# Performance work log

Hardware: AMD Instinct MI355X
Metric: run time of the kernel (lower is better)

Reference implementation:

```python
import jax, jax.numpy as jnp
import numpy as np

OUT_FEATURES = 4096
IN_FEATURES = 4096
GROUP_SIZE = 128
NUM_GROUPS = IN_FEATURES // GROUP_SIZE  # 32
PACKED_SIZE = OUT_FEATURES * IN_FEATURES // 8  # 2097152


def setup_inputs() -> dict:
    key = jax.random.key(0)
    k1, k2, k3, k4 = jax.random.split(key, 4)
    x = jax.random.normal(k1, (2, 512, IN_FEATURES), dtype=jnp.float32)
    # random packed 4-bit weights (8 nibbles per int32)
    w_packed = jax.random.randint(k2, (PACKED_SIZE,), jnp.iinfo(jnp.int32).min,
                                  jnp.iinfo(jnp.int32).max, dtype=jnp.int32)
    w_scale = jax.random.uniform(k3, (OUT_FEATURES, NUM_GROUPS), dtype=jnp.float32) * 0.05
    w_zero = jax.random.randint(k4, (OUT_FEATURES, NUM_GROUPS), 0, 8, dtype=jnp.int32)
    return {"x": x, "w_packed": w_packed, "w_scale": w_scale, "w_zero": w_zero}


def _unpack_dequant(w_packed, w_scale, w_zero):
    # Extract 8 nibbles per int32: (v >> (i*4)) & 0xF, i = 0..7
    shifts = jnp.arange(8, dtype=jnp.int32) * 4
    nibbles = (w_packed[:, None] >> shifts[None, :]) & 15  # [packed, 8]
    w4 = nibbles.reshape(-1)  # [out*in], values 0..15
    w4 = jnp.where(w4 >= 8, w4 - 16, w4)  # signed 4-bit -> [-8, 7]
    w_int = w4.reshape(OUT_FEATURES, NUM_GROUPS, GROUP_SIZE).astype(jnp.float32)
    # per-(row, group) dequant: (q - zero) * scale
    w = (w_int - w_zero[:, :, None].astype(jnp.float32)) * w_scale[:, :, None]
    return w.reshape(OUT_FEATURES, IN_FEATURES)


def reference(x, w_packed, w_scale, w_zero):
    weight = _unpack_dequant(w_packed, w_scale, w_zero).astype(x.dtype)
    # F.linear: y = x @ W^T
    return jnp.einsum('bsi,oi->bso', x, weight)
```

## Files before the change

### kernel.cpp

```cpp
#include <hip/hip_runtime.h>
#include <stdint.h>

#define IN_F 4096
#define OUT_F 4096
#define NG 32
#define NSTEP 32

typedef __attribute__((ext_vector_type(8))) _Float16 half8;
typedef __attribute__((ext_vector_type(2))) _Float16 half2t;
typedef __attribute__((ext_vector_type(4))) float floatx4;

__device__ __forceinline__ unsigned pkh(float a, float b) {
  return __builtin_bit_cast(unsigned, __builtin_amdgcn_cvt_pkrtz(a, b));
}

__global__ __launch_bounds__(256) void prep_kernel(
    const float* __restrict__ x, _Float16* __restrict__ Xh,
    const float* __restrict__ wscale, const int* __restrict__ wzero,
    uint2* __restrict__ SZ, int nxb) {
  int b = blockIdx.x;
  if (b < nxb) {
    int i = b * 256 + threadIdx.x;
    const float4* x4 = (const float4*)x;
    float4 a = x4[2 * i];
    float4 c = x4[2 * i + 1];
    uint4 o;
    o.x = pkh(a.x, c.x);
    o.y = pkh(a.y, c.y);
    o.z = pkh(a.z, c.z);
    o.w = pkh(a.w, c.w);
    ((uint4*)Xh)[i] = o;
  } else {
    int i = (b - nxb) * 256 + threadIdx.x;
    float s = wscale[i];
    int zp = wzero[i];
    _Float16 sh = (_Float16)s;
    _Float16 ch = (_Float16)(float)(1032 + zp);
    unsigned s2 = (unsigned)__builtin_bit_cast(unsigned short, sh) * 0x10001u;
    unsigned c2 = (unsigned)__builtin_bit_cast(unsigned short, ch) * 0x10001u;
    SZ[i] = make_uint2(s2, c2);
  }
}

__device__ __forceinline__ uint4 dequant8(unsigned v, uint2 szv) {
  unsigned tx = v ^ 0x88888888u;
  half2t s2 = __builtin_bit_cast(half2t, szv.x);
  half2t c2 = __builtin_bit_cast(half2t, szv.y);
  unsigned p0 = (tx & 0x000F000Fu) | 0x64006400u;
  unsigned p1 = ((tx >> 4) & 0x000F000Fu) | 0x64006400u;
  unsigned p2 = ((tx >> 8) & 0x000F000Fu) | 0x64006400u;
  unsigned p3 = ((tx >> 12) & 0x000F000Fu) | 0x64006400u;
  half2t w0 = (__builtin_bit_cast(half2t, p0) - c2) * s2;
  half2t w1 = (__builtin_bit_cast(half2t, p1) - c2) * s2;
  half2t w2 = (__builtin_bit_cast(half2t, p2) - c2) * s2;
  half2t w3 = (__builtin_bit_cast(half2t, p3) - c2) * s2;
  uint4 o;
  o.x = __builtin_bit_cast(unsigned, w0);
  o.y = __builtin_bit_cast(unsigned, w1);
  o.z = __builtin_bit_cast(unsigned, w2);
  o.w = __builtin_bit_cast(unsigned, w3);
  return o;
}

__global__ __launch_bounds__(512, 2) void gemm_fused(
    const _Float16* __restrict__ A, const int* __restrict__ wp,
    const uint2* __restrict__ SZ, float* __restrict__ out,
    int M, int N, int K) {
  __shared__ __align__(16) _Float16 Alds[6 * 8192];
  __shared__ __align__(16) _Float16 Blds[4 * 8192];

  const int t = threadIdx.x;
  const int wave = t >> 6, lane = t & 63;
  const int h = wave >> 2, w2 = wave & 3;
  const int wm = (w2 >> 1) * 64, wn = (w2 & 1) * 64;
  const int r = lane & 15, quad = lane >> 4, rb = r & 7;
  const int bm = blockIdx.y * 128, bn = blockIdx.x * 128;

  floatx4 acc[4][4] = {};

  const int kc = t & 7, row0 = t >> 3, row1 = row0 + 64;
  const int gkc = kc ^ (row0 & 7);
  const _Float16* Ag = A + (size_t)bm * K;
  const _Float16* gA[4];
  gA[0] = Ag + (size_t)row0 * K + gkc * 8;
  gA[1] = Ag + (size_t)row1 * K + gkc * 8;
  gA[2] = gA[0] + 2048;
  gA[3] = gA[1] + 2048;

#define STAGE_A(i, st)                                                        \
  {                                                                           \
    _Pragma("unroll") for (int j = 0; j < 4; ++j) {                           \
      const _Float16* src = gA[j] + (i) * 64;                                 \
      int dst = ((st) * 2 + (j >> 1)) * 8192 + (t + 512 * (j & 1)) * 8;       \
      __builtin_amdgcn_global_load_lds(                                       \
          (const __attribute__((address_space(1))) void*)src,                 \
          (__attribute__((address_space(3))) void*)(&Alds[dst]), 16, 0, 0);   \
    }                                                                         \
  }

  const int brow0 = t >> 3, kc8 = t & 7;
  const int* gB0 = wp + (size_t)(bn + brow0) * (IN_F / 8) + kc8;
  const int* gB1 = wp + (size_t)(bn + brow0 + 64) * (IN_F / 8) + kc8;
  const uint2* gS0 = SZ + (size_t)(bn + brow0) * NG;
  const uint2* gS1 = SZ + (size_t)(bn + brow0 + 64) * NG;
  const int bslot0 = brow0 * 64 + ((kc8 ^ (brow0 & 7)) << 3);
  const int bslot1 = (brow0 + 64) * 64 + ((kc8 ^ (brow0 & 7)) << 3);

#define LOADV_B(i, v)                                                         \
  {                                                                           \
    v[0] = (unsigned)gB0[(i) * 8];                                            \
    v[1] = (unsigned)gB1[(i) * 8];                                            \
    v[2] = (unsigned)gB0[(i) * 8 + 256];                                      \
    v[3] = (unsigned)gB1[(i) * 8 + 256];                                      \
  }

#define LOADV_S(g)                                                            \
  {                                                                           \
    sCur[0] = gS0[(g)];                                                       \
    sCur[1] = gS1[(g)];                                                       \
    sCur[2] = gS0[(g) + 16];                                                  \
    sCur[3] = gS1[(g) + 16];                                                  \
  }

#define WRITE_B(v, dstbuf)                                                    \
  {                                                                           \
    _Pragma("unroll") for (int j = 0; j < 4; ++j) {                           \
      int ofs = ((dstbuf) * 2 + (j >> 1)) * 8192 + ((j & 1) ? bslot1 : bslot0); \
      *(uint4*)&Blds[ofs] = dequant8(v[j], sCur[j]);                          \
    }                                                                         \
  }

  unsigned vA[4], vB[4];
  uint2 sCur[4];
  int ra = 0, rw = 2;

  LOADV_B(0, vB);
  LOADV_S(0);
  WRITE_B(vB, 0);
  LOADV_B(1, vA);
  asm volatile("" ::: "memory");
  STAGE_A(0, 0);
  STAGE_A(1, 1);
  asm volatile("s_waitcnt vmcnt(4) lgkmcnt(0)" ::: "memory");
  __builtin_amdgcn_s_barrier();
  __builtin_amdgcn_sched_barrier(0);

#define STEP(i, p, vC, vL, DOSZ, CNTS)                                        \
  {                                                                           \
    if ((i) + 1 < NSTEP) WRITE_B(vC, (p) ^ 1);                                \
    if ((i) + 2 < NSTEP) {                                                    \
      LOADV_B((i) + 2, vL);                                                   \
      if (DOSZ) LOADV_S(((i) + 3) >> 1);                                      \
    }                                                                         \
    asm volatile("" ::: "memory");      \
    if ((i) + 2 < NSTEP) STAGE_A((i) + 2, rw);                                \
    const _Float16* Ab = &Alds[(ra * 2 + h) * 8192];                          \
    const _Float16* Bb = &Blds[((p) * 2 + h) * 8192];                         \
    _Pragma("unroll") for (int ks = 0; ks < 2; ++ks) {                        \
      half8 af[4], bf[4];                                                     \
      _Pragma("unroll") for (int mi = 0; mi < 4; ++mi) {                      \
        int R = wm + mi * 16 + r;                                             \
        af[mi] = *(const half8*)&Ab[R * 64 + (((ks * 4 + quad) ^ rb) << 3)];  \
      }                                                                       \
      _Pragma("unroll") for (int ni = 0; ni < 4; ++ni) {                      \
        int R = wn + ni * 16 + r;                                             \
        bf[ni] = *(const half8*)&Bb[R * 64 + (((ks * 4 + quad) ^ rb) << 3)];  \
      }                                                                       \
      _Pragma("unroll") for (int mi = 0; mi < 4; ++mi)                        \
        _Pragma("unroll") for (int ni = 0; ni < 4; ++ni)                      \
          acc[mi][ni] = __builtin_amdgcn_mfma_f32_16x16x32_f16(               \
              af[mi], bf[ni], acc[mi][ni], 0, 0, 0);                          \
    }                                                                         \
    if ((i) + 2 < NSTEP)                                                      \
      asm volatile("s_waitcnt vmcnt(" CNTS ") lgkmcnt(0)" ::: "memory");      \
    else                                                                      \
      asm volatile("s_waitcnt vmcnt(0) lgkmcnt(0)" ::: "memory");             \
    __builtin_amdgcn_s_barrier();                                             \
    __builtin_amdgcn_sched_barrier(0);                                        \
    ra = (ra + 1 == 3) ? 0 : ra + 1;                                          \
    rw = (rw + 1 == 3) ? 0 : rw + 1;                                          \
  }

  for (int i = 0; i < NSTEP; i += 2) {
    STEP(i, 0, vA, vB, 1, "12");
    STEP(i + 1, 1, vB, vA, 0, "8");
  }

  floatx4* red = (floatx4*)Alds;
  if (h == 1) {
#pragma unroll
    for (int mi = 0; mi < 4; ++mi)
#pragma unroll
      for (int ni = 0; ni < 4; ++ni)
        red[(mi * 4 + ni) * 256 + w2 * 64 + lane] = acc[mi][ni];
  }
  __syncthreads();
  if (h == 0) {
#pragma unroll
    for (int mi = 0; mi < 4; ++mi) {
#pragma unroll
      for (int ni = 0; ni < 4; ++ni) {
        acc[mi][ni] += red[(mi * 4 + ni) * 256 + w2 * 64 + lane];
#pragma unroll
        for (int i = 0; i < 4; ++i) {
          int grow = bm + wm + mi * 16 + quad * 4 + i;
          int gcol = bn + wn + ni * 16 + r;
          out[(size_t)grow * N + gcol] = acc[mi][ni][i];
        }
      }
    }
  }
}

extern "C" void kernel_launch(void* const* d_in, const int* in_sizes, int n_in,
                              void* d_out, int out_size, void* d_ws, size_t ws_size,
                              hipStream_t stream) {
  const float* x = (const float*)d_in[0];
  const int* wp = (const int*)d_in[1];
  const float* wscale = (const float*)d_in[2];
  const int* wzero = (const int*)d_in[3];
  float* out = (float*)d_out;

  int M = in_sizes[0] / IN_F;

  _Float16* Xh = (_Float16*)d_ws;
  uint2* SZ = (uint2*)((char*)d_ws + (size_t)M * IN_F * 2);

  int nxb = (M * IN_F / 8) / 256;
  int nzb = (OUT_F * NG) / 256;
  prep_kernel<<<nxb + nzb, 256, 0, stream>>>(x, Xh, wscale, wzero, SZ, nxb);

  dim3 grid(OUT_F / 128, M / 128);
  gemm_fused<<<grid, 512, 0, stream>>>(Xh, wp, SZ, out, M, OUT_F, IN_F);
}
```

Baseline: 125.8 us.

## Split each K-step into two half-phases with interleaved loads and prioritized MFMA

Each main-loop step is split into two halves. Each half does part of the B dequant write, its LDS fragment loads, part of the global B and A staging, and then 16 MFMAs bracketed by extra barriers and s_setprio(1). This is a ping-pong style schedule meant to overlap memory issue with matrix-core work across waves and raise MFMA priority. It adds two more barriers per step and retunes the vmcnt counts, which risks extra synchronization stalls or subtle ordering errors.

```diff
diff --git a/kernel.cpp b/kernel.cpp
--- a/kernel.cpp
+++ b/kernel.cpp
@@ -87,9 +87,9 @@
   gA[2] = gA[0] + 2048;
   gA[3] = gA[1] + 2048;
 
-#define STAGE_A(i, st)                                                        \
-  {                                                                           \
-    _Pragma("unroll") for (int j = 0; j < 4; ++j) {                           \
+#define STAGE_A_HALF(i, st, hh)                                               \
+  {                                                                           \
+    _Pragma("unroll") for (int j = (hh) * 2; j < (hh) * 2 + 2; ++j) {         \
       const _Float16* src = gA[j] + (i) * 64;                                 \
       int dst = ((st) * 2 + (j >> 1)) * 8192 + (t + 512 * (j & 1)) * 8;       \
       __builtin_amdgcn_global_load_lds(                                       \
@@ -106,14 +106,6 @@
   const int bslot0 = brow0 * 64 + ((kc8 ^ (brow0 & 7)) << 3);
   const int bslot1 = (brow0 + 64) * 64 + ((kc8 ^ (brow0 & 7)) << 3);
 
-#define LOADV_B(i, v)                                                         \
-  {                                                                           \
-    v[0] = (unsigned)gB0[(i) * 8];                                            \
-    v[1] = (unsigned)gB1[(i) * 8];                                            \
-    v[2] = (unsigned)gB0[(i) * 8 + 256];                                      \
-    v[3] = (unsigned)gB1[(i) * 8 + 256];                                      \
-  }
-
 #define LOADV_S(g)                                                            \
   {                                                                           \
     sCur[0] = gS0[(g)];                                                       \
@@ -122,9 +114,9 @@
     sCur[3] = gS1[(g) + 16];                                                  \
   }
 
-#define WRITE_B(v, dstbuf)                                                    \
-  {                                                                           \
-    _Pragma("unroll") for (int j = 0; j < 4; ++j) {                           \
+#define WRITE_B_HALF(v, dstbuf, hh)                                           \
+  {                                                                           \
+    _Pragma("unroll") for (int j = (hh) * 2; j < (hh) * 2 + 2; ++j) {         \
       int ofs = ((dstbuf) * 2 + (j >> 1)) * 8192 + ((j & 1) ? bslot1 : bslot0); \
       *(uint4*)&Blds[ofs] = dequant8(v[j], sCur[j]);                          \
     }                                                                         \
@@ -134,55 +126,97 @@
   uint2 sCur[4];
   int ra = 0, rw = 2;
 
-  LOADV_B(0, vB);
-  LOADV_S(0);
-  WRITE_B(vB, 0);
-  LOADV_B(1, vA);
-  asm volatile("" ::: "memory");
-  STAGE_A(0, 0);
-  STAGE_A(1, 1);
-  asm volatile("s_waitcnt vmcnt(4) lgkmcnt(0)" ::: "memory");
-  __builtin_amdgcn_s_barrier();
-  __builtin_amdgcn_sched_barrier(0);
+  {
+    vB[0] = (unsigned)gB0[0];
+    vB[1] = (unsigned)gB1[0];
+    vB[2] = (unsigned)gB0[256];
+    vB[3] = (unsigned)gB1[256];
+    LOADV_S(0);
+    WRITE_B_HALF(vB, 0, 0);
+    WRITE_B_HALF(vB, 0, 1);
+    vA[0] = (unsigned)gB0[8];
+    vA[1] = (unsigned)gB1[8];
+    vA[2] = (unsigned)gB0[8 + 256];
+    vA[3] = (unsigned)gB1[8 + 256];
+    asm volatile("" ::: "memory");
+    STAGE_A_HALF(0, 0, 0);
+    STAGE_A_HALF(0, 0, 1);
+    STAGE_A_HALF(1, 1, 0);
+    STAGE_A_HALF(1, 1, 1);
+    asm volatile("s_waitcnt vmcnt(4) lgkmcnt(0)" ::: "memory");
+    __builtin_amdgcn_s_barrier();
+    __builtin_amdgcn_sched_barrier(0);
+  }
+
+#define MFMA16(af, bf)                                                        \
+  _Pragma("unroll") for (int mi = 0; mi < 4; ++mi)                            \
+    _Pragma("unroll") for (int ni = 0; ni < 4; ++ni)                          \
+      acc[mi][ni] = __builtin_amdgcn_mfma_f32_16x16x32_f16(                   \
+          af[mi], bf[ni], acc[mi][ni], 0, 0, 0);
 
 #define STEP(i, p, vC, vL, DOSZ, CNTS)                                        \
   {                                                                           \
-    if ((i) + 1 < NSTEP) WRITE_B(vC, (p) ^ 1);                                \
-    if ((i) + 2 < NSTEP) {                                                    \
-      LOADV_B((i) + 2, vL);                                                   \
-      if (DOSZ) LOADV_S(((i) + 3) >> 1);                                      \
-    }                                                                         \
-    asm volatile("" ::: "memory");      \
-    if ((i) + 2 < NSTEP) STAGE_A((i) + 2, rw);                                \
     const _Float16* Ab = &Alds[(ra * 2 + h) * 8192];                          \
     const _Float16* Bb = &Blds[((p) * 2 + h) * 8192];                         \
-    _Pragma("unroll") for (int ks = 0; ks < 2; ++ks) {                        \
-      half8 af[4], bf[4];                                                     \
-      _Pragma("unroll") for (int mi = 0; mi < 4; ++mi) {                      \
-        int R = wm + mi * 16 + r;                                             \
-        af[mi] = *(const half8*)&Ab[R * 64 + (((ks * 4 + quad) ^ rb) << 3)];  \
-      }                                                                       \
-      _Pragma("unroll") for (int ni = 0; ni < 4; ++ni) {                      \
-        int R = wn + ni * 16 + r;                                             \
-        bf[ni] = *(const half8*)&Bb[R * 64 + (((ks * 4 + quad) ^ rb) << 3)];  \
-      }                                                                       \
-      _Pragma("unroll") for (int mi = 0; mi < 4; ++mi)                        \
-        _Pragma("unroll") for (int ni = 0; ni < 4; ++ni)                      \
-          acc[mi][ni] = __builtin_amdgcn_mfma_f32_16x16x32_f16(               \
-              af[mi], bf[ni], acc[mi][ni], 0, 0, 0);                          \
-    }                                                                         \
+                      \
+    if ((i) + 1 < NSTEP) WRITE_B_HALF(vC, (p) ^ 1, 0);                        \
+    half8 af0[4], bf0[4];                                                     \
+    _Pragma("unroll") for (int mi = 0; mi < 4; ++mi) {                        \
+      int R = wm + mi * 16 + r;                                               \
+      af0[mi] = *(const half8*)&Ab[R * 64 + ((quad ^ rb) << 3)];              \
+    }                                                                         \
+    _Pragma("unroll") for (int ni = 0; ni < 4; ++ni) {                        \
+      int R = wn + ni * 16 + r;                                               \
+      bf0[ni] = *(const half8*)&Bb[R * 64 + ((quad ^ rb) << 3)];              \
+    }                                                                         \
+    if ((i) + 2 < NSTEP) {                                                    \
+      vL[0] = (unsigned)gB0[((i) + 2) * 8];                                   \
+      vL[1] = (unsigned)gB1[((i) + 2) * 8];                                   \
+    }                                                                         \
+    asm volatile("" ::: "memory");                                            \
+    if ((i) + 2 < NSTEP) STAGE_A_HALF((i) + 2, rw, 0);                        \
+    __builtin_amdgcn_s_barrier();                                             \
+    asm volatile("s_waitcnt lgkmcnt(0)" ::: "memory");                        \
+    __builtin_amdgcn_sched_barrier(0);                                        \
+    __builtin_amdgcn_s_setprio(1);                                            \
+    MFMA16(af0, bf0);                                                         \
+    __builtin_amdgcn_s_setprio(0);                                            \
+    __builtin_amdgcn_s_barrier();                                             \
+                      \
+    if ((i) + 1 < NSTEP) WRITE_B_HALF(vC, (p) ^ 1, 1);                        \
+    half8 af1[4], bf1[4];                                                     \
+    _Pragma("unroll") for (int mi = 0; mi < 4; ++mi) {                        \
+      int R = wm + mi * 16 + r;                                               \
+      af1[mi] = *(const half8*)&Ab[R * 64 + (((4 + quad) ^ rb) << 3)];        \
+    }                                                                         \
+    _Pragma("unroll") for (int ni = 0; ni < 4; ++ni) {                        \
+      int R = wn + ni * 16 + r;                                               \
+      bf1[ni] = *(const half8*)&Bb[R * 64 + (((4 + quad) ^ rb) << 3)];        \
+    }                                                                         \
+    if ((i) + 2 < NSTEP) {                                                    \
+      vL[2] = (unsigned)gB0[((i) + 2) * 8 + 256];                             \
+      vL[3] = (unsigned)gB1[((i) + 2) * 8 + 256];                             \
+      if (DOSZ) LOADV_S(((i) + 3) >> 1);       \
+    }                                                                         \
+    asm volatile("" ::: "memory");                                            \
+    if ((i) + 2 < NSTEP) STAGE_A_HALF((i) + 2, rw, 1);                        \
     if ((i) + 2 < NSTEP)                                                      \
-      asm volatile("s_waitcnt vmcnt(" CNTS ") lgkmcnt(0)" ::: "memory");      \
+      asm volatile("s_waitcnt vmcnt(" CNTS ")" ::: "memory");                 \
     else                                                                      \
-      asm volatile("s_waitcnt vmcnt(0) lgkmcnt(0)" ::: "memory");             \
-    __builtin_amdgcn_s_barrier();                                             \
+      asm volatile("s_waitcnt vmcnt(0)" ::: "memory");                        \
+    __builtin_amdgcn_s_barrier();                                             \
+    asm volatile("s_waitcnt lgkmcnt(0)" ::: "memory");                        \
     __builtin_amdgcn_sched_barrier(0);                                        \
+    __builtin_amdgcn_s_setprio(1);                                            \
+    MFMA16(af1, bf1);                                                         \
+    __builtin_amdgcn_s_setprio(0);                                            \
+    __builtin_amdgcn_s_barrier();                                             \
     ra = (ra + 1 == 3) ? 0 : ra + 1;                                          \
     rw = (rw + 1 == 3) ? 0 : rw + 1;                                          \
   }
 
   for (int i = 0; i < NSTEP; i += 2) {
-    STEP(i, 0, vA, vB, 1, "12");
+    STEP(i, 0, vA, vB, 1, "10");
     STEP(i + 1, 1, vB, vA, 0, "8");
   }
 
```

Result: no change. 124.2 us (-1.3%).

## Store packed 4-bit weights in LDS and dequantize at fragment load time

Applied to the files above, without the earlier changes.

Instead of dequantizing weights to fp16 before writing them to LDS, the kernel now stores the raw packed int32 nibbles in LDS and dequantizes each B fragment in registers right before the MFMA. This cuts B LDS footprint and write traffic by a factor of four. It also changes the pipeline from a 3-stage A ring with hand-tuned waitcnts to a simple double buffer with __syncthreads. The cost is redundant dequant ALU work, since every wave that reads a B fragment recomputes it. The simpler synchronization may also expose more memory latency.

```diff
diff --git a/kernel.cpp b/kernel.cpp
--- a/kernel.cpp
+++ b/kernel.cpp
@@ -42,7 +42,7 @@
   }
 }
 
-__device__ __forceinline__ uint4 dequant8(unsigned v, uint2 szv) {
+__device__ __forceinline__ half8 dequant8(unsigned v, uint2 szv) {
   unsigned tx = v ^ 0x88888888u;
   half2t s2 = __builtin_bit_cast(half2t, szv.x);
   half2t c2 = __builtin_bit_cast(half2t, szv.y);
@@ -59,15 +59,15 @@
   o.y = __builtin_bit_cast(unsigned, w1);
   o.z = __builtin_bit_cast(unsigned, w2);
   o.w = __builtin_bit_cast(unsigned, w3);
-  return o;
+  return __builtin_bit_cast(half8, o);
 }
 
 __global__ __launch_bounds__(512, 2) void gemm_fused(
     const _Float16* __restrict__ A, const int* __restrict__ wp,
     const uint2* __restrict__ SZ, float* __restrict__ out,
     int M, int N, int K) {
-  __shared__ __align__(16) _Float16 Alds[6 * 8192];
-  __shared__ __align__(16) _Float16 Blds[4 * 8192];
+  __shared__ __align__(16) _Float16 Alds[4 * 8192];
+  __shared__ unsigned Bpk[2 * 2 * 1024];
 
   const int t = threadIdx.x;
   const int wave = t >> 6, lane = t & 63;
@@ -87,11 +87,11 @@
   gA[2] = gA[0] + 2048;
   gA[3] = gA[1] + 2048;
 
-#define STAGE_A(i, st)                                                        \
+#define STAGE_A(i, buf)                                                       \
   {                                                                           \
     _Pragma("unroll") for (int j = 0; j < 4; ++j) {                           \
       const _Float16* src = gA[j] + (i) * 64;                                 \
-      int dst = ((st) * 2 + (j >> 1)) * 8192 + (t + 512 * (j & 1)) * 8;       \
+      int dst = ((j >> 1) * 2 + (buf)) * 8192 + (t + 512 * (j & 1)) * 8;      \
       __builtin_amdgcn_global_load_lds(                                       \
           (const __attribute__((address_space(1))) void*)src,                 \
           (__attribute__((address_space(3))) void*)(&Alds[dst]), 16, 0, 0);   \
@@ -101,10 +101,7 @@
   const int brow0 = t >> 3, kc8 = t & 7;
   const int* gB0 = wp + (size_t)(bn + brow0) * (IN_F / 8) + kc8;
   const int* gB1 = wp + (size_t)(bn + brow0 + 64) * (IN_F / 8) + kc8;
-  const uint2* gS0 = SZ + (size_t)(bn + brow0) * NG;
-  const uint2* gS1 = SZ + (size_t)(bn + brow0 + 64) * NG;
-  const int bslot0 = brow0 * 64 + ((kc8 ^ (brow0 & 7)) << 3);
-  const int bslot1 = (brow0 + 64) * 64 + ((kc8 ^ (brow0 & 7)) << 3);
+  const int bsl = kc8 ^ (brow0 & 7);
 
 #define LOADV_B(i, v)                                                         \
   {                                                                           \
@@ -114,76 +111,78 @@
     v[3] = (unsigned)gB1[(i) * 8 + 256];                                      \
   }
 
-#define LOADV_S(g)                                                            \
-  {                                                                           \
-    sCur[0] = gS0[(g)];                                                       \
-    sCur[1] = gS1[(g)];                                                       \
-    sCur[2] = gS0[(g) + 16];                                                  \
-    sCur[3] = gS1[(g) + 16];                                                  \
-  }
-
-#define WRITE_B(v, dstbuf)                                                    \
-  {                                                                           \
-    _Pragma("unroll") for (int j = 0; j < 4; ++j) {                           \
-      int ofs = ((dstbuf) * 2 + (j >> 1)) * 8192 + ((j & 1) ? bslot1 : bslot0); \
-      *(uint4*)&Blds[ofs] = dequant8(v[j], sCur[j]);                          \
-    }                                                                         \
-  }
-
-  unsigned vA[4], vB[4];
-  uint2 sCur[4];
-  int ra = 0, rw = 2;
-
-  LOADV_B(0, vB);
-  LOADV_S(0);
-  WRITE_B(vB, 0);
-  LOADV_B(1, vA);
-  asm volatile("" ::: "memory");
-  STAGE_A(0, 0);
-  STAGE_A(1, 1);
-  asm volatile("s_waitcnt vmcnt(4) lgkmcnt(0)" ::: "memory");
-  __builtin_amdgcn_s_barrier();
-  __builtin_amdgcn_sched_barrier(0);
-
-#define STEP(i, p, vC, vL, DOSZ, CNTS)                                        \
-  {                                                                           \
-    if ((i) + 1 < NSTEP) WRITE_B(vC, (p) ^ 1);                                \
-    if ((i) + 2 < NSTEP) {                                                    \
-      LOADV_B((i) + 2, vL);                                                   \
-      if (DOSZ) LOADV_S(((i) + 3) >> 1);                                      \
-    }                                                                         \
-    asm volatile("" ::: "memory");      \
-    if ((i) + 2 < NSTEP) STAGE_A((i) + 2, rw);                                \
-    const _Float16* Ab = &Alds[(ra * 2 + h) * 8192];                          \
-    const _Float16* Bb = &Blds[((p) * 2 + h) * 8192];                         \
+#define WRITE_BP(v, buf)                                                      \
+  {                                                                           \
+    unsigned* b0 = &Bpk[((buf) * 2 + 0) * 1024];                              \
+    unsigned* b1 = &Bpk[((buf) * 2 + 1) * 1024];                              \
+    b0[brow0 * 8 + bsl] = v[0];                                               \
+    b0[(brow0 + 64) * 8 + bsl] = v[1];                                        \
+    b1[brow0 * 8 + bsl] = v[2];                                               \
+    b1[(brow0 + 64) * 8 + bsl] = v[3];                                        \
+  }
+
+  const uint2* gSc[4];
+#pragma unroll
+  for (int ni = 0; ni < 4; ++ni)
+    gSc[ni] = SZ + (size_t)(bn + wn + ni * 16 + r) * NG + h * 16;
+
+#define LOADV_S(dst, p)                                                       \
+  {                                                                           \
+    _Pragma("unroll") for (int ni = 0; ni < 4; ++ni) dst[ni] = gSc[ni][(p)];  \
+  }
+
+#define COMPUTE(buf, szp)                                                     \
+  {                                                                           \
+    const _Float16* Ab = &Alds[(h * 2 + (buf)) * 8192];                       \
+    const unsigned* Bb = &Bpk[((buf) * 2 + h) * 1024];                        \
     _Pragma("unroll") for (int ks = 0; ks < 2; ++ks) {                        \
       half8 af[4], bf[4];                                                     \
       _Pragma("unroll") for (int mi = 0; mi < 4; ++mi) {                      \
         int R = wm + mi * 16 + r;                                             \
-        af[mi] = *(const half8*)&Ab[R * 64 + (((ks * 4 + quad) ^ rb) << 3)];  \
+        af[mi] = *(const half8*)&Alds[(h * 2 + (buf)) * 8192 + R * 64 +       \
+                                      (((ks * 4 + quad) ^ rb) << 3)];         \
       }                                                                       \
       _Pragma("unroll") for (int ni = 0; ni < 4; ++ni) {                      \
         int R = wn + ni * 16 + r;                                             \
-        bf[ni] = *(const half8*)&Bb[R * 64 + (((ks * 4 + quad) ^ rb) << 3)];  \
+        unsigned bq = Bb[R * 8 + ((ks * 4 + quad) ^ rb)];                     \
+        bf[ni] = dequant8(bq, szp[ni]);                                       \
       }                                                                       \
       _Pragma("unroll") for (int mi = 0; mi < 4; ++mi)                        \
         _Pragma("unroll") for (int ni = 0; ni < 4; ++ni)                      \
           acc[mi][ni] = __builtin_amdgcn_mfma_f32_16x16x32_f16(               \
               af[mi], bf[ni], acc[mi][ni], 0, 0, 0);                          \
     }                                                                         \
-    if ((i) + 2 < NSTEP)                                                      \
-      asm volatile("s_waitcnt vmcnt(" CNTS ") lgkmcnt(0)" ::: "memory");      \
-    else                                                                      \
-      asm volatile("s_waitcnt vmcnt(0) lgkmcnt(0)" ::: "memory");             \
-    __builtin_amdgcn_s_barrier();                                             \
-    __builtin_amdgcn_sched_barrier(0);                                        \
-    ra = (ra + 1 == 3) ? 0 : ra + 1;                                          \
-    rw = (rw + 1 == 3) ? 0 : rw + 1;                                          \
-  }
-
-  for (int i = 0; i < NSTEP; i += 2) {
-    STEP(i, 0, vA, vB, 1, "12");
-    STEP(i + 1, 1, vB, vA, 0, "8");
+  }
+
+  unsigned vA[4], vB[4];
+  uint2 szA[4], szB[4];
+
+  LOADV_B(0, vA);
+  LOADV_S(szA, 0);
+  STAGE_A(0, 0);
+  WRITE_BP(vA, 0);
+  LOADV_B(1, vB);
+  __syncthreads();
+
+  for (int i = 0; i < NSTEP; i += 4) {
+    if (i + 1 < NSTEP) { STAGE_A(i + 1, 1); WRITE_BP(vB, 1); }
+    if (i + 2 < NSTEP) LOADV_B(i + 2, vA);
+    COMPUTE(0, szA);
+    __syncthreads();
+    if (i + 2 < NSTEP) { STAGE_A(i + 2, 0); WRITE_BP(vA, 0); }
+    if (i + 3 < NSTEP) LOADV_B(i + 3, vB);
+    if (i + 2 < NSTEP) LOADV_S(szB, (i + 2) >> 1);
+    COMPUTE(1, szA);
+    __syncthreads();
+    if (i + 3 < NSTEP) { STAGE_A(i + 3, 1); WRITE_BP(vB, 1); }
+    if (i + 4 < NSTEP) LOADV_B(i + 4, vA);
+    COMPUTE(0, szB);
+    __syncthreads();
+    if (i + 4 < NSTEP) { STAGE_A(i + 4, 0); WRITE_BP(vA, 0); }
+    if (i + 5 < NSTEP) LOADV_B(i + 5, vB);
+    if (i + 4 < NSTEP) LOADV_S(szA, (i + 4) >> 1);
+    COMPUTE(1, szB);
+    __syncthreads();
   }
 
   floatx4* red = (floatx4*)Alds;
@@ -202,10 +201,10 @@
       for (int ni = 0; ni < 4; ++ni) {
         acc[mi][ni] += red[(mi * 4 + ni) * 256 + w2 * 64 + lane];
 #pragma unroll
-        for (int i = 0; i < 4; ++i) {
-          int grow = bm + wm + mi * 16 + quad * 4 + i;
+        for (int i2 = 0; i2 < 4; ++i2) {
+          int grow = bm + wm + mi * 16 + quad * 4 + i2;
           int gcol = bn + wn + ni * 16 + r;
-          out[(size_t)grow * N + gcol] = acc[mi][ni][i];
+          out[(size_t)grow * N + gcol] = acc[mi][ni][i2];
         }
       }
     }
```

Measured after the change: 137.2 us. +9.1%, slower.
